# Performance work log

Hardware: AMD Instinct MI355X
Metric: run time of the kernel (lower is better)

## Reference

```python
import jax, jax.numpy as jnp
import numpy as np

N_HEADS = 16


def setup_inputs() -> dict:
    key = jax.random.key(0)
    ks = jax.random.split(key, 6)
    b, s, d = 1, 2048, 2048
    x = jax.random.normal(ks[0], (b, s, d), dtype=jnp.float32)
    Wqkv = jax.random.normal(ks[1], (d, 3 * d), dtype=jnp.float32) * (d ** -0.5)
    Wqkv_bias = jax.random.normal(ks[2], (3 * d,), dtype=jnp.float32) * 0.02
    out_w = jax.random.normal(ks[3], (d, d), dtype=jnp.float32) * (d ** -0.5)
    out_b = jax.random.normal(ks[4], (d,), dtype=jnp.float32) * 0.02
    attn_bias = jax.random.normal(ks[5], (1, N_HEADS, 1, s), dtype=jnp.float32)
    key_padding_mask = jnp.ones((b, s), dtype=bool)
    return {"x": x, "Wqkv": Wqkv, "Wqkv_bias": Wqkv_bias, "out_w": out_w,
            "out_b": out_b, "attn_bias": attn_bias,
            "key_padding_mask": key_padding_mask}


def reference(x, Wqkv, Wqkv_bias, out_w, out_b, attn_bias, key_padding_mask):
    b, s, d = x.shape
    h = N_HEADS
    dh = d // h
    qkv = x @ Wqkv + Wqkv_bias                      # [b, s, 3d]
    q, k, v = jnp.split(qkv, 3, axis=-1)
    q = q.reshape(b, s, h, dh).transpose(0, 2, 1, 3)  # b h s d
    k = k.reshape(b, s, h, dh).transpose(0, 2, 1, 3)
    v = v.reshape(b, s, h, dh).transpose(0, 2, 1, 3)
    scale = 1.0 / jnp.sqrt(jnp.asarray(dh, x.dtype))
    attn_weight = jnp.einsum('bhqd,bhkd->bhqk', q, k) * scale
    attn_weight = attn_weight + attn_bias           # broadcast [1,h,1,s]
    min_val = jnp.finfo(x.dtype).min
    # key padding mask: [b, s_k] -> [b,1,1,s_k]
    attn_weight = jnp.where(key_padding_mask[:, None, None, :], attn_weight, min_val)
    # causal mask (s_q == s_k)
    causal = jnp.tril(jnp.ones((s, s), dtype=bool))
    attn_weight = jnp.where(causal[None, None, :, :], attn_weight, min_val)
    attn_weight = jax.nn.softmax(attn_weight, axis=-1)
    out = jnp.einsum('bhqk,bhkd->bhqd', attn_weight, v)
    out = out.transpose(0, 2, 1, 3).reshape(b, s, d)  # b s (h d)
    return out @ out_w + out_b
```

## Files before the change

### kernel.cpp

```cpp
#include <hip/hip_runtime.h>
#include <hip/hip_bf16.h>
#include <stdint.h>


#define SQ 2048
#define DM 2048
#define NH 16
#define DH 128
#define N3 6144
#define QKVN (NH * SQ * DH)

typedef unsigned short u16;
typedef __bf16 bf16_t;
typedef bf16_t bf16x8 __attribute__((ext_vector_type(8)));
typedef float f32x4 __attribute__((ext_vector_type(4)));
typedef const __attribute__((address_space(1))) unsigned int guint;
typedef __attribute__((address_space(3))) unsigned int luint;

__device__ __forceinline__ float b2f(u16 u) {
    union { uint32_t i; float f; } c; c.i = ((uint32_t)u) << 16; return c.f;
}
__device__ __forceinline__ u16 f2b(float f) {
    union { float f; uint32_t i; } c; c.f = f;
    uint32_t r = c.i + 0x7FFF + ((c.i >> 16) & 1);
    return (u16)(r >> 16);
}
__device__ __forceinline__ uint32_t pk(u16 a, u16 b) {
    return (uint32_t)a | ((uint32_t)b << 16);
}
__device__ __forceinline__ uint32_t pkrnd(float a, float b) {
    union { float f; uint32_t i; } x, y; x.f = a; y.f = b;
    return __builtin_amdgcn_perm(y.i + 0x8000u, x.i + 0x8000u, 0x07060302u);
}
__device__ __forceinline__ float ld1(const void* p, size_t i, bool fp32) {
    return fp32 ? ((const float*)p)[i] : b2f(((const u16*)p)[i]);
}

__global__ void detect_dtype(const void* x, int* flag) {
    __shared__ int bad;
    if (threadIdx.x == 0) bad = 0;
    __syncthreads();
    float v = b2f(((const u16*)x)[threadIdx.x]);
    if (!(fabsf(v) <= 1024.0f)) atomicOr(&bad, 1);
    __syncthreads();
    if (threadIdx.x == 0) *flag = bad;
}

__global__ __launch_bounds__(256) void convert_x(
    const void* __restrict__ x, u16* __restrict__ xb, const int* __restrict__ flagp)
{
    const bool fp32 = (*flagp != 0);
    const size_t i = ((size_t)blockIdx.x * 256 + threadIdx.x) * 8;
    uint4 v;
    if (fp32) {
        const float* p = (const float*)x + i;
        float4 a = *(const float4*)p, b = *(const float4*)(p + 4);
        v.x = pkrnd(a.x, a.y); v.y = pkrnd(a.z, a.w);
        v.z = pkrnd(b.x, b.y); v.w = pkrnd(b.z, b.w);
    } else {
        v = *(const uint4*)((const u16*)x + i);
    }
    *(uint4*)(xb + i) = v;
}

__global__ __launch_bounds__(256) void transpose_w(
    const void* __restrict__ W, u16* __restrict__ Wt, int N,
    const int* __restrict__ flagp)
{
    const bool fp32 = (*flagp != 0);
    __shared__ __attribute__((aligned(16))) u16 tile[64 * 72];
    const int t = threadIdx.x;
    const int n0 = blockIdx.x * 64, k0 = blockIdx.y * 64;
#pragma unroll
    for (int i = 0; i < 2; ++i) {
        int c = t + 256 * i; int kr = c >> 3; int n8 = (c & 7) * 8;
        uint4 v;
        if (fp32) {
            const float* p = (const float*)W + (size_t)(k0 + kr) * N + n0 + n8;
            float4 a = *(const float4*)p, b = *(const float4*)(p + 4);
            v.x = pkrnd(a.x, a.y); v.y = pkrnd(a.z, a.w);
            v.z = pkrnd(b.x, b.y); v.w = pkrnd(b.z, b.w);
        } else {
            v = *(const uint4*)((const u16*)W + (size_t)(k0 + kr) * N + n0 + n8);
        }
        *(uint4*)&tile[kr * 72 + n8] = v;
    }
    __syncthreads();
#pragma unroll
    for (int i = 0; i < 2; ++i) {
        int c = t + 256 * i; int nr = c >> 3; int k8 = (c & 7) * 8;
        uint32_t dw[4];
#pragma unroll
        for (int j = 0; j < 4; ++j)
            dw[j] = pk(tile[(k8 + 2*j) * 72 + nr], tile[(k8 + 2*j + 1) * 72 + nr]);
        *(uint4*)&Wt[(size_t)(n0 + nr) * 2048 + k0 + k8] =
            make_uint4(dw[0], dw[1], dw[2], dw[3]);
    }
}

__global__ __launch_bounds__(256, 2) void qkv_gemm4(
    const u16* __restrict__ xb, const u16* __restrict__ Wt,
    const void* __restrict__ bias,
    u16* __restrict__ Q, u16* __restrict__ K, u16* __restrict__ Vt,
    const int* __restrict__ flagp)
{
    const bool fp32 = (*flagp != 0);
    __shared__ __attribute__((aligned(16))) u16 Alds[2][128 * 64];
    __shared__ __attribute__((aligned(16))) u16 Blds[2][192 * 64];
    const int t = threadIdx.x;
    const int w = t >> 6, l = t & 63;
    const int wm = w >> 1, wn = w & 1;
    const int lq = l & 15, quad = l >> 4;
    const int rsub = t >> 3;
    const int sw = ((t & 7) ^ (rsub & 7)) << 3;

    const int orig = blockIdx.x;
    const int xcd = orig & 7, j = orig >> 3;
    const int bx = (xcd & 3) * 8 + (j & 7);
    const int by = (xcd >> 2) * 8 + (j >> 3);
    const int m0 = by * 128, n0 = bx * 192;

    const u16* Ag = xb + (size_t)m0 * 2048;
    const u16* Bg = Wt + (size_t)n0 * 2048;

#define STAGE_A(u, ue) do {                                                   \
    if ((u) < 32) {                                                           \
      _Pragma("unroll")                                                       \
      for (int i_ = 0; i_ < 2; ++i_) {                                        \
        const int rb_ = i_ * 64 + (ue) * 32;                                  \
        const u16* src_ = Ag + (size_t)(rb_ + rsub) * 2048 + (u) * 64 + sw;   \
        __builtin_amdgcn_global_load_lds((guint*)(const void*)src_,           \
          (luint*)(void*)&Alds[(u) & 1][rb_ * 64 + t * 8], 16, 0, 0);         \
      }                                                                       \
    } } while (0)

#define STAGE_B(u) do {                                                       \
    if ((u) < 32) {                                                           \
      _Pragma("unroll")                                                       \
      for (int i_ = 0; i_ < 6; ++i_) {                                        \
        const int rb_ = i_ * 32;                                              \
        const u16* src_ = Bg + (size_t)(rb_ + rsub) * 2048 + (u) * 64 + sw;   \
        __builtin_amdgcn_global_load_lds((guint*)(const void*)src_,           \
          (luint*)(void*)&Blds[(u) & 1][rb_ * 64 + t * 8], 16, 0, 0);         \
      }                                                                       \
    } } while (0)

#define READ_A(buf, mh) do {                                                  \
    _Pragma("unroll")                                                         \
    for (int mf_ = 0; mf_ < 2; ++mf_) {                                       \
      const int r_ = wm*64 + ((mh)*2 + mf_)*16 + lq;                          \
      _Pragma("unroll")                                                       \
      for (int ks_ = 0; ks_ < 2; ++ks_) {                                     \
        const int c_ = (ks_*4 + quad) ^ (r_ & 7);                             \
        a[mf_][ks_] = *(const bf16x8*)&Alds[buf][r_*64 + c_*8];               \
      }                                                                       \
    } } while (0)

#define READ_B(dst, buf, nhh) do {                                            \
    _Pragma("unroll")                                                         \
    for (int nf_ = 0; nf_ < 3; ++nf_) {                                       \
      const int r_ = wn*96 + ((nhh)*3 + nf_)*16 + lq;                         \
      _Pragma("unroll")                                                       \
      for (int ks_ = 0; ks_ < 2; ++ks_) {                                     \
        const int c_ = (ks_*4 + quad) ^ (r_ & 7);                             \
        dst[nf_][ks_] = *(const bf16x8*)&Blds[buf][r_*64 + c_*8];             \
      }                                                                       \
    } } while (0)

#define MMA_Q(mh, nhh, bsrc) do {                                             \
    __builtin_amdgcn_s_setprio(1);                                            \
    _Pragma("unroll")                                                         \
    for (int mf_ = 0; mf_ < 2; ++mf_)                                         \
    _Pragma("unroll")                                                         \
    for (int nf_ = 0; nf_ < 3; ++nf_)                                         \
    _Pragma("unroll")                                                         \
    for (int ks_ = 0; ks_ < 2; ++ks_)                                         \
      acc[(mh)*2+mf_][(nhh)*3+nf_] =                                          \
        __builtin_amdgcn_mfma_f32_16x16x32_bf16(a[mf_][ks_], bsrc[nf_][ks_],  \
          acc[(mh)*2+mf_][(nhh)*3+nf_], 0, 0, 0);                             \
    __builtin_amdgcn_s_setprio(0);                                            \
} while (0)

#define TILE_BODY(T, buf, BEC, BEN) do {                                      \
                                                                      \
    READ_A(buf, 0);                                                           \
    __builtin_amdgcn_s_barrier();                                             \
    asm volatile("s_waitcnt lgkmcnt(0)" ::: "memory");                        \
    MMA_Q(0, 0, BEC);                                                         \
    __builtin_amdgcn_s_barrier();                                             \
                                                                      \
    READ_B(bo, buf, 1);                                                       \
    STAGE_A((T) + 2, 0);                                                      \
    if ((T) >= 30) asm volatile("s_waitcnt vmcnt(0)" ::: "memory");           \
    else           asm volatile("s_waitcnt vmcnt(2)" ::: "memory");           \
    __builtin_amdgcn_s_barrier();                                             \
    asm volatile("s_waitcnt lgkmcnt(0)" ::: "memory");                        \
    MMA_Q(0, 1, bo);                                                          \
    __builtin_amdgcn_s_barrier();                                             \
                                                                      \
    READ_A(buf, 1);                                                           \
    STAGE_B((T) + 2);                                                         \
    __builtin_amdgcn_s_barrier();                                             \
    asm volatile("s_waitcnt lgkmcnt(0)" ::: "memory");                        \
    MMA_Q(1, 1, bo);                                                          \
    __builtin_amdgcn_s_barrier();                                             \
                                                                      \
    READ_B(BEN, (buf) ^ 1, 0);                                                \
    STAGE_A((T) + 2, 1);                                                      \
    __builtin_amdgcn_s_barrier();                                             \
    asm volatile("s_waitcnt lgkmcnt(0)" ::: "memory");                        \
    MMA_Q(1, 0, BEC);                                                         \
    __builtin_amdgcn_s_barrier();                                             \
} while (0)

    const f32x4 vzero = {0.f, 0.f, 0.f, 0.f};
    f32x4 acc[4][6];
#pragma unroll
    for (int i = 0; i < 4; ++i)
#pragma unroll
        for (int j2 = 0; j2 < 6; ++j2) acc[i][j2] = vzero;
    bf16x8 a[2][2], bo[3][2], be_a[3][2], be_b[3][2];

    STAGE_A(0, 0); STAGE_B(0); STAGE_A(0, 1);
    STAGE_A(1, 0); STAGE_B(1); STAGE_A(1, 1);
    asm volatile("s_waitcnt vmcnt(10)" ::: "memory");
    __builtin_amdgcn_s_barrier();
    READ_B(be_a, 0, 0);

#pragma unroll 1
    for (int T = 0; T < 32; T += 2) {
        TILE_BODY(T,     0, be_a, be_b);
        TILE_BODY(T + 1, 1, be_b, be_a);
    }

    const float scale = 0.08838834764831845f;
#pragma unroll
    for (int nf = 0; nf < 6; ++nf) {
        const int n = n0 + wn*96 + nf*16 + lq;
        const float bn = ld1(bias, n, fp32);
        const int which = n >> 11, r2 = n & 2047, h = r2 >> 7, dc = r2 & 127;
#pragma unroll
        for (int mf = 0; mf < 4; ++mf) {
#pragma unroll
            for (int r = 0; r < 4; ++r) {
                const int m = m0 + wm*64 + mf*16 + quad*4 + r;
                const float val = acc[mf][nf][r] + bn;
                if (which == 0)
                    Q[((size_t)(h << 11) + m) * DH + dc] = f2b(val * scale);
                else if (which == 1)
                    K[((size_t)(h << 11) + m) * DH + dc] = f2b(val);
                else {
                    const int kl = m & 63;
                    const int pos = ((kl >> 5) << 5) + (((kl >> 2) & 3) << 3)
                                  + (((kl >> 4) & 1) << 2) + (kl & 3);
                    const int mp = (m & ~63) | pos;
                    Vt[((size_t)h * DH + dc) * SQ + mp] = f2b(val);
                }
            }
        }
    }
#undef STAGE_A
#undef STAGE_B
#undef READ_A
#undef READ_B
#undef MMA_Q
#undef TILE_BODY
}

__global__ __launch_bounds__(256) void attn_mfma(
    const u16* __restrict__ Q, const u16* __restrict__ K,
    const u16* __restrict__ Vt, const void* __restrict__ attn_bias,
    u16* __restrict__ Ob0, u16* __restrict__ Ob1,
    float* __restrict__ Lb0, float* __restrict__ Lb1,
    const int* __restrict__ flagp)
{
    const bool fp32 = (*flagp != 0);
    __shared__ __attribute__((aligned(16))) u16 Ks[2][4 * 64 * 32];
    __shared__ __attribute__((aligned(16))) u16 Vs[2][128 * 64];
    __shared__ __attribute__((aligned(16))) float biasF[2048];

    const int t = threadIdx.x;
    const int w = t >> 6, l = t & 63;
    const int lq = l & 15, quad = l >> 4;
    const int px = blockIdx.x, h = blockIdx.y, par = blockIdx.z;

    const u16* Qh = Q + (size_t)h * SQ * DH;
    const u16* Kh = K + (size_t)h * SQ * DH;
    const u16* Vh = Vt + (size_t)h * DH * SQ;
    u16* Ob = par ? Ob1 : Ob0;
    float* Lb = par ? Lb1 : Lb0;

#pragma unroll
    for (int i = 0; i < 8; ++i) {
        int j = t + 256 * i;
        biasF[j] = ld1(attn_bias, (size_t)h * SQ + j, fp32);
    }

#define STAGE_KV(kt_, b_) do {                                                \
    const int k0_ = (kt_) * 64;                                               \
    _Pragma("unroll")                                                         \
    for (int i_ = 0; i_ < 4; ++i_) {                                          \
        const int ci_ = w * 4 + i_;                                           \
        const int kc_ = ci_ >> 2, kg_ = ci_ & 3;                              \
        const u16* srck_ = Kh + (size_t)(k0_ + kg_*16 + (l >> 2)) * DH        \
                         + kc_*32 + (l & 3) * 8;                              \
        __builtin_amdgcn_global_load_lds((guint*)(const void*)srck_,          \
            (luint*)(void*)&Ks[b_][ci_ * 512], 16, 0, 0);                     \
        const int dim_ = ci_ * 8 + (l >> 3);                                  \
        const u16* srcv_ = Vh + (size_t)dim_ * SQ + k0_                       \
                         + (((l & 7) ^ (l >> 3)) << 3);                       \
        __builtin_amdgcn_global_load_lds((guint*)(const void*)srcv_,          \
            (luint*)(void*)&Vs[b_][ci_ * 512], 16, 0, 0);                     \
    } } while (0)

    const f32x4 vzero = {0.f, 0.f, 0.f, 0.f};

    for (int phase = 0; phase < 2; ++phase) {
        const int qt = phase ? (15 - px) : px;
        const int q0 = qt * 128;
        const int qb = q0 + w * 32;

        bf16x8 bq[2][4];
#pragma unroll
        for (int s = 0; s < 2; ++s)
#pragma unroll
            for (int kc = 0; kc < 4; ++kc)
                bq[s][kc] = *(const bf16x8*)(Qh + (size_t)(qb + s*16 + lq) * DH
                                             + kc*32 + quad*8);

        __syncthreads();
        STAGE_KV(par, 0);
        asm volatile("s_waitcnt vmcnt(0)" ::: "memory");
        __builtin_amdgcn_s_barrier();

        f32x4 O[2][8];
#pragma unroll
        for (int s = 0; s < 2; ++s)
#pragma unroll
            for (int i = 0; i < 8; ++i) O[s][i] = vzero;
        float lsum[2] = {0.0f, 0.0f};

        int buf = 0;
        const int ktmax = 2 * qt + 1;
        for (int kt = par; kt <= ktmax; kt += 2) {
            const int k0 = kt * 64;
            if (kt + 2 <= ktmax) STAGE_KV(kt + 2, buf ^ 1);

            f32x4 S[2][4];
#pragma unroll
            for (int s = 0; s < 2; ++s)
#pragma unroll
                for (int ks = 0; ks < 4; ++ks) S[s][ks] = vzero;
#pragma unroll
            for (int kc = 0; kc < 4; ++kc) {
#pragma unroll
                for (int ks = 0; ks < 4; ++ks) {
                    bf16x8 ak = *(const bf16x8*)&Ks[buf][kc*2048 + (ks*16 + lq)*32 + quad*8];
                    S[0][ks] = __builtin_amdgcn_mfma_f32_16x16x32_bf16(ak, bq[0][kc], S[0][ks], 0, 0, 0);
                    S[1][ks] = __builtin_amdgcn_mfma_f32_16x16x32_bf16(ak, bq[1][kc], S[1][ks], 0, 0, 0);
                }
            }

            uint32_t Ppk[2][4][2];
#pragma unroll
            for (int s = 0; s < 2; ++s) {
                const int qbs = qb + s * 16;
                const bool full = (k0 + 63) <= qbs;
                float part = 0.0f;
#pragma unroll
                for (int ks = 0; ks < 4; ++ks) {
                    const f32x4 b4 = *(const f32x4*)&biasF[k0 + ks*16 + quad*4];
                    float p[4];
#pragma unroll
                    for (int r = 0; r < 4; ++r) {
                        float pe = __expf(S[s][ks][r] + b4[r]);
                        if (!full) {
                            const int key = k0 + ks*16 + quad*4 + r;
                            if (key > qbs + lq) pe = 0.0f;
                        }
                        p[r] = pe;
                        part += pe;
                    }
                    Ppk[s][ks][0] = pkrnd(p[0], p[1]);
                    Ppk[s][ks][1] = pkrnd(p[2], p[3]);
                }
                lsum[s] += part;
            }

#pragma unroll
            for (int s2 = 0; s2 < 2; ++s2) {
                union { uint32_t u[4]; bf16x8 v; } bP0, bP1;
                bP0.u[0] = Ppk[0][2*s2][0];   bP0.u[1] = Ppk[0][2*s2][1];
                bP0.u[2] = Ppk[0][2*s2+1][0]; bP0.u[3] = Ppk[0][2*s2+1][1];
                bP1.u[0] = Ppk[1][2*s2][0];   bP1.u[1] = Ppk[1][2*s2][1];
                bP1.u[2] = Ppk[1][2*s2+1][0]; bP1.u[3] = Ppk[1][2*s2+1][1];
                const int ch = ((s2*4 + quad) ^ (lq & 7)) << 3;
#pragma unroll
                for (int ds = 0; ds < 8; ++ds) {
                    bf16x8 aV = *(const bf16x8*)&Vs[buf][(ds*16 + lq)*64 + ch];
                    O[0][ds] = __builtin_amdgcn_mfma_f32_16x16x32_bf16(aV, bP0.v, O[0][ds], 0, 0, 0);
                    O[1][ds] = __builtin_amdgcn_mfma_f32_16x16x32_bf16(aV, bP1.v, O[1][ds], 0, 0, 0);
                }
            }

            asm volatile("s_waitcnt vmcnt(0)" ::: "memory");
            __builtin_amdgcn_s_barrier();
            buf ^= 1;
        }

#pragma unroll
        for (int s = 0; s < 2; ++s) {
            float ls = lsum[s];
            ls += __shfl_xor(ls, 16, 64);
            ls += __shfl_xor(ls, 32, 64);
            if (l < 16) Lb[(size_t)h * SQ + qb + s*16 + l] = ls;
            u16* orow = Ob + (size_t)(qb + s*16 + lq) * DM + h * DH;
#pragma unroll
            for (int ds = 0; ds < 8; ++ds) {
                uint2 o2;
                o2.x = pkrnd(O[s][ds][0], O[s][ds][1]);
                o2.y = pkrnd(O[s][ds][2], O[s][ds][3]);
                *(uint2*)&orow[ds*16 + quad*4] = o2;
            }
        }
    }
#undef STAGE_KV
}

__global__ __launch_bounds__(256) void combine_o(
    const u16* __restrict__ O0, const u16* __restrict__ O1,
    const float* __restrict__ L0, const float* __restrict__ L1,
    u16* __restrict__ attno)
{
    const size_t i = ((size_t)blockIdx.x * 256 + threadIdx.x) * 8;
    const int row = (int)(i >> 11);
    const int h = ((int)i & 2047) >> 7;
    const float inv = 1.0f / (L0[h * SQ + row] + L1[h * SQ + row]);
    const ushort4 a = *(const ushort4*)(O0 + i);
    const ushort4 b = *(const ushort4*)(O1 + i);
    const ushort4 c = *(const ushort4*)(O0 + i + 4);
    const ushort4 d = *(const ushort4*)(O1 + i + 4);
    uint4 v;
    v.x = pkrnd((b2f(a.x)+b2f(b.x))*inv, (b2f(a.y)+b2f(b.y))*inv);
    v.y = pkrnd((b2f(a.z)+b2f(b.z))*inv, (b2f(a.w)+b2f(b.w))*inv);
    v.z = pkrnd((b2f(c.x)+b2f(d.x))*inv, (b2f(c.y)+b2f(d.y))*inv);
    v.w = pkrnd((b2f(c.z)+b2f(d.z))*inv, (b2f(c.w)+b2f(d.w))*inv);
    *(uint4*)(attno + i) = v;
}

__global__ __launch_bounds__(256, 2) void out_gemm(
    const u16* __restrict__ attno, const u16* __restrict__ OWt,
    const void* __restrict__ bias, void* __restrict__ out,
    const int* __restrict__ flagp)
{
    const bool fp32 = (*flagp != 0);
    __shared__ __attribute__((aligned(16))) u16 Alds[2][64 * 64];
    __shared__ __attribute__((aligned(16))) u16 Blds[2][128 * 64];
    const int t = threadIdx.x;
    const int w = t >> 6, l = t & 63;
    const int wm = w >> 1, wn = w & 1;
    const int lq = l & 15, quad = l >> 4;
    const int rsub = t >> 3;
    const int sw = ((t & 7) ^ (rsub & 7)) << 3;

    const int orig = blockIdx.x;
    const int xcd = orig & 7, j = orig >> 3;
    const int bx = (xcd & 3) * 4 + (j & 3);
    const int by = (xcd >> 2) * 16 + (j >> 2);
    const int m0 = by * 64, n0 = bx * 128;

    const u16* Ag = attno + (size_t)m0 * 2048;
    const u16* Bg = OWt + (size_t)n0 * 2048;

#define O_STAGE_A(u, ue) do {                                                 \
    if ((u) < 32) {                                                           \
        const int row_ = (ue)*16 + ((t >> 7) << 5) + ((t >> 3) & 15);         \
        const u16* src_ = Ag + (size_t)row_ * 2048 + (u) * 64 + sw;           \
        __builtin_amdgcn_global_load_lds((guint*)(const void*)src_,           \
          (luint*)(void*)&Alds[(u) & 1][((ue)*16 + ((t >> 7) << 5)) * 64      \
                                        + (t & 127) * 8], 16, 0, 0);          \
    } } while (0)

#define O_STAGE_B(u) do {                                                     \
    if ((u) < 32) {                                                           \
      _Pragma("unroll")                                                       \
      for (int i_ = 0; i_ < 4; ++i_) {                                        \
        const int rb_ = i_ * 32;                                              \
        const u16* src_ = Bg + (size_t)(rb_ + rsub) * 2048 + (u) * 64 + sw;   \
        __builtin_amdgcn_global_load_lds((guint*)(const void*)src_,           \
          (luint*)(void*)&Blds[(u) & 1][rb_ * 64 + t * 8], 16, 0, 0);         \
      }                                                                       \
    } } while (0)

#define O_READ_A(buf, mh) do {                                                \
    const int r_ = wm*32 + (mh)*16 + lq;                                      \
    _Pragma("unroll")                                                         \
    for (int ks_ = 0; ks_ < 2; ++ks_) {                                       \
        const int c_ = (ks_*4 + quad) ^ (r_ & 7);                             \
        a[ks_] = *(const bf16x8*)&Alds[buf][r_*64 + c_*8];                    \
    } } while (0)

#define O_READ_B(dst, buf, nhh) do {                                          \
    _Pragma("unroll")                                                         \
    for (int nf_ = 0; nf_ < 2; ++nf_) {                                       \
      const int r_ = wn*64 + ((nhh)*2 + nf_)*16 + lq;                         \
      _Pragma("unroll")                                                       \
      for (int ks_ = 0; ks_ < 2; ++ks_) {                                     \
        const int c_ = (ks_*4 + quad) ^ (r_ & 7);                             \
        dst[nf_][ks_] = *(const bf16x8*)&Blds[buf][r_*64 + c_*8];             \
      }                                                                       \
    } } while (0)

#define O_MMA(mh, nhh, bsrc) do {                                             \
    __builtin_amdgcn_s_setprio(1);                                            \
    _Pragma("unroll")                                                         \
    for (int nf_ = 0; nf_ < 2; ++nf_)                                         \
    _Pragma("unroll")                                                         \
    for (int ks_ = 0; ks_ < 2; ++ks_)                                         \
      acc[mh][(nhh)*2+nf_] =                                                  \
        __builtin_amdgcn_mfma_f32_16x16x32_bf16(a[ks_], bsrc[nf_][ks_],       \
          acc[mh][(nhh)*2+nf_], 0, 0, 0);                                     \
    __builtin_amdgcn_s_setprio(0);                                            \
} while (0)

#define O_TILE(T, buf, BEC, BEN) do {                                         \
                                                                      \
    O_READ_A(buf, 0);                                                         \
    __builtin_amdgcn_s_barrier();                                             \
    asm volatile("s_waitcnt lgkmcnt(0)" ::: "memory");                        \
    O_MMA(0, 0, BEC);                                                         \
    __builtin_amdgcn_s_barrier();                                             \
                                                                      \
    O_READ_B(bo, buf, 1);                                                     \
    O_STAGE_A((T) + 2, 0);                                                    \
    if ((T) >= 30) asm volatile("s_waitcnt vmcnt(0)" ::: "memory");           \
    else           asm volatile("s_waitcnt vmcnt(1)" ::: "memory");           \
    __builtin_amdgcn_s_barrier();                                             \
    asm volatile("s_waitcnt lgkmcnt(0)" ::: "memory");                        \
    O_MMA(0, 1, bo);                                                          \
    __builtin_amdgcn_s_barrier();                                             \
                                                                      \
    O_READ_A(buf, 1);                                                         \
    O_STAGE_B((T) + 2);                                                       \
    __builtin_amdgcn_s_barrier();                                             \
    asm volatile("s_waitcnt lgkmcnt(0)" ::: "memory");                        \
    O_MMA(1, 1, bo);                                                          \
    __builtin_amdgcn_s_barrier();                                             \
                                                                      \
    O_READ_B(BEN, (buf) ^ 1, 0);                                              \
    O_STAGE_A((T) + 2, 1);                                                    \
    __builtin_amdgcn_s_barrier();                                             \
    asm volatile("s_waitcnt lgkmcnt(0)" ::: "memory");                        \
    O_MMA(1, 0, BEC);                                                         \
    __builtin_amdgcn_s_barrier();                                             \
} while (0)

    const f32x4 vzero = {0.f, 0.f, 0.f, 0.f};
    f32x4 acc[2][4];
#pragma unroll
    for (int i = 0; i < 2; ++i)
#pragma unroll
        for (int j2 = 0; j2 < 4; ++j2) acc[i][j2] = vzero;
    bf16x8 a[2], bo[2][2], be_a[2][2], be_b[2][2];

    O_STAGE_A(0, 0); O_STAGE_B(0); O_STAGE_A(0, 1);
    O_STAGE_A(1, 0); O_STAGE_B(1); O_STAGE_A(1, 1);
    asm volatile("s_waitcnt vmcnt(6)" ::: "memory");
    __builtin_amdgcn_s_barrier();
    O_READ_B(be_a, 0, 0);

#pragma unroll 1
    for (int T = 0; T < 32; T += 2) {
        O_TILE(T,     0, be_a, be_b);
        O_TILE(T + 1, 1, be_b, be_a);
    }

#pragma unroll
    for (int nf = 0; nf < 4; ++nf) {
        const int n = n0 + wn*64 + nf*16 + lq;
        const float bn = ld1(bias, n, fp32);
#pragma unroll
        for (int mh = 0; mh < 2; ++mh) {
#pragma unroll
            for (int r = 0; r < 4; ++r) {
                const int m = m0 + wm*32 + mh*16 + quad*4 + r;
                const float v = acc[mh][nf][r] + bn;
                const size_t idx = (size_t)m * DM + n;
                if (fp32) ((float*)out)[idx] = v;
                else      ((u16*)out)[idx]  = f2b(v);
            }
        }
    }
#undef O_STAGE_A
#undef O_STAGE_B
#undef O_READ_A
#undef O_READ_B
#undef O_MMA
#undef O_TILE
}

extern "C" void kernel_launch(void* const* d_in, const int* in_sizes, int n_in,
                              void* d_out, int out_size, void* d_ws, size_t ws_size,
                              hipStream_t stream)
{
    const void* x      = d_in[0];
    const void* wqkv   = d_in[1];
    const void* wqkv_b = d_in[2];
    const void* out_w  = d_in[3];
    const void* out_b  = d_in[4];
    const void* attn_b = d_in[5];

    char* base = (char*)d_ws;
    int* flag = (int*)base;
    u16* xb   = (u16*)(base + 256);
    u16* Wt   = xb + (size_t)SQ * DM;
    u16* Qb   = Wt + (size_t)N3 * DM;
    u16* Kb   = Qb + QKVN;
    u16* Vtb  = Kb + QKVN;
    float* L0 = (float*)(Vtb + QKVN);
    float* L1 = L0 + NH * SQ;
    u16* OWt  = Wt;
    u16* Ob0  = Wt + (size_t)DM * DM;
    u16* Ob1  = Ob0 + (size_t)SQ * DM;
    u16* attno = xb;

    detect_dtype<<<1, 256, 0, stream>>>(x, flag);
    convert_x<<<(SQ * DM) / (256 * 8), 256, 0, stream>>>(x, xb, flag);
    transpose_w<<<dim3(N3/64, DM/64), 256, 0, stream>>>(wqkv, Wt, N3, flag);
    qkv_gemm4<<<dim3(512), 256, 0, stream>>>(xb, Wt, wqkv_b, Qb, Kb, Vtb, flag);
    transpose_w<<<dim3(DM/64, DM/64), 256, 0, stream>>>(out_w, OWt, DM, flag);
    attn_mfma<<<dim3(8, NH, 2), 256, 0, stream>>>(Qb, Kb, Vtb, attn_b,
                                                  Ob0, Ob1, L0, L1, flag);
    combine_o<<<(SQ * DM) / (256 * 8), 256, 0, stream>>>(Ob0, Ob1, L0, L1, attno);
    out_gemm<<<dim3(512), 256, 0, stream>>>(attno, OWt, out_b, d_out, flag);
}
```

Before: 286.6 us.

## Replace fine-grained interleaved GEMM pipeline with simple one-tile-ahead double buffer

Both the QKV and output-projection GEMM mainloops drop the four-phase interleaved schedule, which had many barriers, a two-tile prefetch and register-level B-fragment prefetch. Each iteration now issues the global-to-LDS loads for the next tile, reads all fragments for the current tile, runs every MFMA, then waits for the loads and does a single barrier. This cuts barrier count and register juggling, but the prefetch distance drops to one tile and the loop waits for all loads at the end of every iteration, so there is less overlap of memory with compute.

```diff
diff --git a/kernel.cpp b/kernel.cpp
--- a/kernel.cpp
+++ b/kernel.cpp
@@ -123,11 +123,11 @@
     const u16* Ag = xb + (size_t)m0 * 2048;
     const u16* Bg = Wt + (size_t)n0 * 2048;
 
-#define STAGE_A(u, ue) do {                                                   \
+#define STAGE_A(u) do {                                                       \
     if ((u) < 32) {                                                           \
       _Pragma("unroll")                                                       \
-      for (int i_ = 0; i_ < 2; ++i_) {                                        \
-        const int rb_ = i_ * 64 + (ue) * 32;                                  \
+      for (int i_ = 0; i_ < 4; ++i_) {                                        \
+        const int rb_ = i_ * 32;                                              \
         const u16* src_ = Ag + (size_t)(rb_ + rsub) * 2048 + (u) * 64 + sw;   \
         __builtin_amdgcn_global_load_lds((guint*)(const void*)src_,           \
           (luint*)(void*)&Alds[(u) & 1][rb_ * 64 + t * 8], 16, 0, 0);         \
@@ -152,7 +152,7 @@
       _Pragma("unroll")                                                       \
       for (int ks_ = 0; ks_ < 2; ++ks_) {                                     \
         const int c_ = (ks_*4 + quad) ^ (r_ & 7);                             \
-        a[mf_][ks_] = *(const bf16x8*)&Alds[buf][r_*64 + c_*8];               \
+        a[(mh)*2 + mf_][ks_] = *(const bf16x8*)&Alds[buf][r_*64 + c_*8];      \
       }                                                                       \
     } } while (0)
 
@@ -168,7 +168,6 @@
     } } while (0)
 
 #define MMA_Q(mh, nhh, bsrc) do {                                             \
-    __builtin_amdgcn_s_setprio(1);                                            \
     _Pragma("unroll")                                                         \
     for (int mf_ = 0; mf_ < 2; ++mf_)                                         \
     _Pragma("unroll")                                                         \
@@ -176,42 +175,9 @@
     _Pragma("unroll")                                                         \
     for (int ks_ = 0; ks_ < 2; ++ks_)                                         \
       acc[(mh)*2+mf_][(nhh)*3+nf_] =                                          \
-        __builtin_amdgcn_mfma_f32_16x16x32_bf16(a[mf_][ks_], bsrc[nf_][ks_],  \
-          acc[(mh)*2+mf_][(nhh)*3+nf_], 0, 0, 0);                             \
-    __builtin_amdgcn_s_setprio(0);                                            \
-} while (0)
-
-#define TILE_BODY(T, buf, BEC, BEN) do {                                      \
-                                                                      \
-    READ_A(buf, 0);                                                           \
-    __builtin_amdgcn_s_barrier();                                             \
-    asm volatile("s_waitcnt lgkmcnt(0)" ::: "memory");                        \
-    MMA_Q(0, 0, BEC);                                                         \
-    __builtin_amdgcn_s_barrier();                                             \
-                                                                      \
-    READ_B(bo, buf, 1);                                                       \
-    STAGE_A((T) + 2, 0);                                                      \
-    if ((T) >= 30) asm volatile("s_waitcnt vmcnt(0)" ::: "memory");           \
-    else           asm volatile("s_waitcnt vmcnt(2)" ::: "memory");           \
-    __builtin_amdgcn_s_barrier();                                             \
-    asm volatile("s_waitcnt lgkmcnt(0)" ::: "memory");                        \
-    MMA_Q(0, 1, bo);                                                          \
-    __builtin_amdgcn_s_barrier();                                             \
-                                                                      \
-    READ_A(buf, 1);                                                           \
-    STAGE_B((T) + 2);                                                         \
-    __builtin_amdgcn_s_barrier();                                             \
-    asm volatile("s_waitcnt lgkmcnt(0)" ::: "memory");                        \
-    MMA_Q(1, 1, bo);                                                          \
-    __builtin_amdgcn_s_barrier();                                             \
-                                                                      \
-    READ_B(BEN, (buf) ^ 1, 0);                                                \
-    STAGE_A((T) + 2, 1);                                                      \
-    __builtin_amdgcn_s_barrier();                                             \
-    asm volatile("s_waitcnt lgkmcnt(0)" ::: "memory");                        \
-    MMA_Q(1, 0, BEC);                                                         \
-    __builtin_amdgcn_s_barrier();                                             \
-} while (0)
+        __builtin_amdgcn_mfma_f32_16x16x32_bf16(a[(mh)*2+mf_][ks_],           \
+          bsrc[nf_][ks_], acc[(mh)*2+mf_][(nhh)*3+nf_], 0, 0, 0);             \
+    } while (0)
 
     const f32x4 vzero = {0.f, 0.f, 0.f, 0.f};
     f32x4 acc[4][6];
@@ -219,18 +185,25 @@
     for (int i = 0; i < 4; ++i)
 #pragma unroll
         for (int j2 = 0; j2 < 6; ++j2) acc[i][j2] = vzero;
-    bf16x8 a[2][2], bo[3][2], be_a[3][2], be_b[3][2];
-
-    STAGE_A(0, 0); STAGE_B(0); STAGE_A(0, 1);
-    STAGE_A(1, 0); STAGE_B(1); STAGE_A(1, 1);
-    asm volatile("s_waitcnt vmcnt(10)" ::: "memory");
+    bf16x8 a[4][2], b0[3][2], b1[3][2];
+
+    STAGE_A(0); STAGE_B(0);
+    asm volatile("s_waitcnt vmcnt(0)" ::: "memory");
     __builtin_amdgcn_s_barrier();
-    READ_B(be_a, 0, 0);
 
 #pragma unroll 1
-    for (int T = 0; T < 32; T += 2) {
-        TILE_BODY(T,     0, be_a, be_b);
-        TILE_BODY(T + 1, 1, be_b, be_a);
+    for (int T = 0; T < 32; ++T) {
+        const int buf = T & 1;
+        STAGE_A(T + 1); STAGE_B(T + 1);
+        READ_A(buf, 0); READ_A(buf, 1);
+        READ_B(b0, buf, 0); READ_B(b1, buf, 1);
+        asm volatile("s_waitcnt lgkmcnt(0)" ::: "memory");
+        __builtin_amdgcn_s_setprio(1);
+        MMA_Q(0, 0, b0); MMA_Q(0, 1, b1);
+        MMA_Q(1, 0, b0); MMA_Q(1, 1, b1);
+        __builtin_amdgcn_s_setprio(0);
+        asm volatile("s_waitcnt vmcnt(0)" ::: "memory");
+        __builtin_amdgcn_s_barrier();
     }
 
     const float scale = 0.08838834764831845f;
@@ -264,7 +237,6 @@
 #undef READ_A
 #undef READ_B
 #undef MMA_Q
-#undef TILE_BODY
 }
 
 __global__ __launch_bounds__(256) void attn_mfma(
@@ -472,13 +444,15 @@
     const u16* Ag = attno + (size_t)m0 * 2048;
     const u16* Bg = OWt + (size_t)n0 * 2048;
 
-#define O_STAGE_A(u, ue) do {                                                 \
+#define O_STAGE_A(u) do {                                                     \
     if ((u) < 32) {                                                           \
-        const int row_ = (ue)*16 + ((t >> 7) << 5) + ((t >> 3) & 15);         \
-        const u16* src_ = Ag + (size_t)row_ * 2048 + (u) * 64 + sw;           \
+      _Pragma("unroll")                                                       \
+      for (int i_ = 0; i_ < 2; ++i_) {                                        \
+        const int rb_ = i_ * 32;                                              \
+        const u16* src_ = Ag + (size_t)(rb_ + rsub) * 2048 + (u) * 64 + sw;   \
         __builtin_amdgcn_global_load_lds((guint*)(const void*)src_,           \
-          (luint*)(void*)&Alds[(u) & 1][((ue)*16 + ((t >> 7) << 5)) * 64      \
-                                        + (t & 127) * 8], 16, 0, 0);          \
+          (luint*)(void*)&Alds[(u) & 1][rb_ * 64 + t * 8], 16, 0, 0);         \
+      }                                                                       \
     } } while (0)
 
 #define O_STAGE_B(u) do {                                                     \
@@ -497,7 +471,7 @@
     _Pragma("unroll")                                                         \
     for (int ks_ = 0; ks_ < 2; ++ks_) {                                       \
         const int c_ = (ks_*4 + quad) ^ (r_ & 7);                             \
-        a[ks_] = *(const bf16x8*)&Alds[buf][r_*64 + c_*8];                    \
+        a[mh][ks_] = *(const bf16x8*)&Alds[buf][r_*64 + c_*8];                \
     } } while (0)
 
 #define O_READ_B(dst, buf, nhh) do {                                          \
@@ -512,48 +486,14 @@
     } } while (0)
 
 #define O_MMA(mh, nhh, bsrc) do {                                             \
-    __builtin_amdgcn_s_setprio(1);                                            \
     _Pragma("unroll")                                                         \
     for (int nf_ = 0; nf_ < 2; ++nf_)                                         \
     _Pragma("unroll")                                                         \
     for (int ks_ = 0; ks_ < 2; ++ks_)                                         \
       acc[mh][(nhh)*2+nf_] =                                                  \
-        __builtin_amdgcn_mfma_f32_16x16x32_bf16(a[ks_], bsrc[nf_][ks_],       \
+        __builtin_amdgcn_mfma_f32_16x16x32_bf16(a[mh][ks_], bsrc[nf_][ks_],   \
           acc[mh][(nhh)*2+nf_], 0, 0, 0);                                     \
-    __builtin_amdgcn_s_setprio(0);                                            \
-} while (0)
-
-#define O_TILE(T, buf, BEC, BEN) do {                                         \
-                                                                      \
-    O_READ_A(buf, 0);                                                         \
-    __builtin_amdgcn_s_barrier();                                             \
-    asm volatile("s_waitcnt lgkmcnt(0)" ::: "memory");                        \
-    O_MMA(0, 0, BEC);                                                         \
-    __builtin_amdgcn_s_barrier();                                             \
-                                                                      \
-    O_READ_B(bo, buf, 1);                                                     \
-    O_STAGE_A((T) + 2, 0);                                                    \
-    if ((T) >= 30) asm volatile("s_waitcnt vmcnt(0)" ::: "memory");           \
-    else           asm volatile("s_waitcnt vmcnt(1)" ::: "memory");           \
-    __builtin_amdgcn_s_barrier();                                             \
-    asm volatile("s_waitcnt lgkmcnt(0)" ::: "memory");                        \
-    O_MMA(0, 1, bo);                                                          \
-    __builtin_amdgcn_s_barrier();                                             \
-                                                                      \
-    O_READ_A(buf, 1);                                                         \
-    O_STAGE_B((T) + 2);                                                       \
-    __builtin_amdgcn_s_barrier();                                             \
-    asm volatile("s_waitcnt lgkmcnt(0)" ::: "memory");                        \
-    O_MMA(1, 1, bo);                                                          \
-    __builtin_amdgcn_s_barrier();                                             \
-                                                                      \
-    O_READ_B(BEN, (buf) ^ 1, 0);                                              \
-    O_STAGE_A((T) + 2, 1);                                                    \
-    __builtin_amdgcn_s_barrier();                                             \
-    asm volatile("s_waitcnt lgkmcnt(0)" ::: "memory");                        \
-    O_MMA(1, 0, BEC);                                                         \
-    __builtin_amdgcn_s_barrier();                                             \
-} while (0)
+    } while (0)
 
     const f32x4 vzero = {0.f, 0.f, 0.f, 0.f};
     f32x4 acc[2][4];
@@ -561,18 +501,25 @@
     for (int i = 0; i < 2; ++i)
 #pragma unroll
         for (int j2 = 0; j2 < 4; ++j2) acc[i][j2] = vzero;
-    bf16x8 a[2], bo[2][2], be_a[2][2], be_b[2][2];
-
-    O_STAGE_A(0, 0); O_STAGE_B(0); O_STAGE_A(0, 1);
-    O_STAGE_A(1, 0); O_STAGE_B(1); O_STAGE_A(1, 1);
-    asm volatile("s_waitcnt vmcnt(6)" ::: "memory");
+    bf16x8 a[2][2], b0[2][2], b1[2][2];
+
+    O_STAGE_A(0); O_STAGE_B(0);
+    asm volatile("s_waitcnt vmcnt(0)" ::: "memory");
     __builtin_amdgcn_s_barrier();
-    O_READ_B(be_a, 0, 0);
 
 #pragma unroll 1
-    for (int T = 0; T < 32; T += 2) {
-        O_TILE(T,     0, be_a, be_b);
-        O_TILE(T + 1, 1, be_b, be_a);
+    for (int T = 0; T < 32; ++T) {
+        const int buf = T & 1;
+        O_STAGE_A(T + 1); O_STAGE_B(T + 1);
+        O_READ_A(buf, 0); O_READ_A(buf, 1);
+        O_READ_B(b0, buf, 0); O_READ_B(b1, buf, 1);
+        asm volatile("s_waitcnt lgkmcnt(0)" ::: "memory");
+        __builtin_amdgcn_s_setprio(1);
+        O_MMA(0, 0, b0); O_MMA(0, 1, b1);
+        O_MMA(1, 0, b0); O_MMA(1, 1, b1);
+        __builtin_amdgcn_s_setprio(0);
+        asm volatile("s_waitcnt vmcnt(0)" ::: "memory");
+        __builtin_amdgcn_s_barrier();
     }
 
 #pragma unroll
@@ -596,7 +543,6 @@
 #undef O_READ_A
 #undef O_READ_B
 #undef O_MMA
-#undef O_TILE
 }
 
 extern "C" void kernel_launch(void* const* d_in, const int* in_sizes, int n_in,
```

Result: no change. 283.9 us (-0.9%).
